# Performance work log

Measured on AMD Instinct MI355X. Metric: run time of the kernel, lower is better.

The kernel has to match this reference:

```python
import jax, jax.numpy as jnp
import numpy as np

# Model config (matches init_kwargs)
B, J, D_IN, D_MODEL, NUM_HEADS, NUM_LAYERS = 1024, 24, 64, 512, 8, 6
A = J + 1  # joints + cls token
LN_EPS = 1e-5


def setup_inputs() -> dict:
    key = jax.random.key(0)
    ks = jax.random.split(key, 14)
    s = 0.02  # weight init scale
    return {
        "x": jax.random.normal(ks[0], (B, J, D_IN), dtype=jnp.float32),
        # per-joint input embeddings: Linear(d_in, d_model) x J
        "We": jax.random.normal(ks[1], (J, D_IN, D_MODEL), dtype=jnp.float32) * s,
        "be": jnp.zeros((J, D_MODEL), dtype=jnp.float32),
        "cls_token": jax.random.normal(ks[2], (D_MODEL,), dtype=jnp.float32),
        # per-layer shared key/value projections
        "Wk": jax.random.normal(ks[3], (NUM_LAYERS, D_MODEL, D_MODEL), dtype=jnp.float32) * s,
        "bk": jnp.zeros((NUM_LAYERS, D_MODEL), dtype=jnp.float32),
        "Wv": jax.random.normal(ks[4], (NUM_LAYERS, D_MODEL, D_MODEL), dtype=jnp.float32) * s,
        "bv": jnp.zeros((NUM_LAYERS, D_MODEL), dtype=jnp.float32),
        # per-layer, PER-JOINT query projections (ModuleList of A linears)
        "Wq": jax.random.normal(ks[5], (NUM_LAYERS, A, D_MODEL, D_MODEL), dtype=jnp.float32) * s,
        "bq": jnp.zeros((NUM_LAYERS, A, D_MODEL), dtype=jnp.float32),
        "Wo": jax.random.normal(ks[6], (NUM_LAYERS, D_MODEL, D_MODEL), dtype=jnp.float32) * s,
        "bo": jnp.zeros((NUM_LAYERS, D_MODEL), dtype=jnp.float32),
        "ln_g": jnp.ones((NUM_LAYERS, D_MODEL), dtype=jnp.float32),
        "ln_b": jnp.zeros((NUM_LAYERS, D_MODEL), dtype=jnp.float32),
    }


def _layernorm(y, g, b):
    m = jnp.mean(y, axis=-1, keepdims=True)
    v = jnp.var(y, axis=-1, keepdims=True)  # ddof=0 matches torch LayerNorm
    return (y - m) * jax.lax.rsqrt(v + LN_EPS) * g + b


def reference(x, We, be, cls_token, Wk, bk, Wv, bv, Wq, bq, Wo, bo, ln_g, ln_b):
    b = x.shape[0]
    depth = D_MODEL // NUM_HEADS
    # per-joint input embedding -> (B, J, D)
    tok = jnp.einsum("bjd,jde->bje", x, We) + be
    cls = jnp.broadcast_to(cls_token[None, None, :], (b, 1, D_MODEL))
    h = jnp.concatenate([cls, tok], axis=1)  # (B, A, D); the seq dim of 1 is dropped

    def split(t):  # (B, A, D) -> (B, H, A, depth)
        return t.reshape(b, A, NUM_HEADS, depth).transpose(0, 2, 1, 3)

    for l in range(NUM_LAYERS):
        k = h @ Wk[l] + bk[l]                                  # (B, A, D)
        v = h @ Wv[l] + bv[l]                                  # (B, A, D)
        q = jnp.einsum("bad,ade->bae", h, Wq[l]) + bq[l]        # per-joint query
        qh, kh, vh = split(q), split(k), split(v)
        scores = jnp.einsum("bhqd,bhkd->bhqk", qh, kh) / jnp.sqrt(jnp.float32(depth))
        w = jax.nn.softmax(scores, axis=-1)                    # (B, H, A, A)
        o = jnp.einsum("bhqk,bhkd->bhqd", w, vh)
        o = o.transpose(0, 2, 1, 3).reshape(b, A, D_MODEL)
        o = o @ Wo[l] + bo[l]
        h = _layernorm(h + o, ln_g[l], ln_b[l])
    return h  # (B, A, D) == inputs[:, 0, :, :] in the torch code
```

## Files before the change

### kernel.cpp

```cpp
#include <hip/hip_runtime.h>

typedef unsigned short u16;
typedef unsigned int u32;
typedef short bf16x8 __attribute__((ext_vector_type(8)));
typedef float f32x4 __attribute__((ext_vector_type(4)));

#define AS1 __attribute__((address_space(1)))
#define AS3 __attribute__((address_space(3)))

__device__ __forceinline__ u16 f2b(float f) {
  u32 u = __float_as_uint(f);
  u += 0x7fffu + ((u >> 16) & 1u);
  return (u16)(u >> 16);
}
__device__ __forceinline__ float b2f(u16 s) {
  return __uint_as_float(((u32)s) << 16);
}

__device__ __forceinline__ void gload16(const u16* g, u16* l) {
  __builtin_amdgcn_global_load_lds((const AS1 void*)g, (AS3 void*)l, 16, 0, 0);
}

__global__ __launch_bounds__(256) void prep_kernel(const float* __restrict__ x,
                                                   const float* __restrict__ cls,
                                                   u16* __restrict__ xb,
                                                   u16* __restrict__ hb) {
  if (blockIdx.x < 1536) {
    int i = blockIdx.x * 256 + threadIdx.x;
    float4 v = ((const float4*)x)[i];
    ushort4 u;
    u.x = f2b(v.x); u.y = f2b(v.y); u.z = f2b(v.z); u.w = f2b(v.w);
    ((ushort4*)xb)[i] = u;
  } else {
    int i = (blockIdx.x - 1536) * 256 + threadIdx.x;
    int b = i >> 7;
    int e = (i & 127) << 2;
    float4 v = *(const float4*)(cls + e);
    long off = (long)b * (25 * 512) + e;
    ushort4 u;
    u.x = f2b(v.x); u.y = f2b(v.y); u.z = f2b(v.z); u.w = f2b(v.w);
    *(ushort4*)(hb + off) = u;
  }
}

__device__ __forceinline__ void conv_tile(const float* __restrict__ src,
                                          u16* __restrict__ dst,
                                          int K, int N, int k0, int n0,
                                          void* smem) {
  float (*t)[65] = (float(*)[65])smem;
  for (int i = threadIdx.x; i < 4096; i += 256) {
    int r = i >> 6, c = i & 63;
    t[r][c] = src[(long)(k0 + r) * N + n0 + c];
  }
  __syncthreads();
  for (int i = threadIdx.x; i < 4096; i += 256) {
    int r = i >> 6, c = i & 63;
    dst[(long)(n0 + r) * K + k0 + c] = f2b(t[c][r]);
  }
}

__global__ __launch_bounds__(256) void convT_kernel(const float* __restrict__ src,
                                                    u16* __restrict__ dst,
                                                    int K, int N,
                                                    long src_gstride, long dst_gstride) {
  __shared__ float t[64][65];
  conv_tile(src + (long)blockIdx.z * src_gstride, dst + (long)blockIdx.z * dst_gstride,
            K, N, blockIdx.x * 64, blockIdx.y * 64, t);
}

__global__ __launch_bounds__(256) void convT4_kernel(
    const float* __restrict__ wq, const float* __restrict__ wk,
    const float* __restrict__ wv, const float* __restrict__ wo,
    u16* __restrict__ dq, u16* __restrict__ dk,
    u16* __restrict__ dv, u16* __restrict__ dwo) {
  __shared__ float t[64][65];
  const int z = blockIdx.z;
  const float* src;
  u16* dst;
  if (z < 25)      { src = wq + (long)z * 262144; dst = dq + (long)z * 262144; }
  else if (z == 25){ src = wk; dst = dk; }
  else if (z == 26){ src = wv; dst = dv; }
  else             { src = wo; dst = dwo; }
  conv_tile(src, dst, 512, 512, blockIdx.x * 64, blockIdx.y * 64, t);
}

__device__ __forceinline__ void gemm_core(u16* lds,
    const u16* Ag, long a_stride, const u16* Wg, const float* biasg,
    u16* Cg, long c_stride, int K, int m0, int n0) {
  u16* As = lds;
  u16* Bs = lds + 8192;

  const int tid = threadIdx.x;
  const int lane = tid & 63;
  const int wave = tid >> 6;
  const int wr = wave >> 1, wc = wave & 1;

  const int schunk = lane & 7;
  const u16* ga[4];
  const u16* gb[4];
  int lo[4];
#pragma unroll
  for (int i = 0; i < 4; ++i) {
    const int r = wave * 32 + i * 8 + (lane >> 3);
    const int csw = (schunk ^ (r & 7)) << 3;
    ga[i] = Ag + (long)(m0 + r) * a_stride + csw;
    gb[i] = Wg + (long)(n0 + r) * K + csw;
    lo[i] = (wave * 32 + i * 8) * 64;
  }

  f32x4 acc[4][4];
#pragma unroll
  for (int m = 0; m < 4; ++m)
#pragma unroll
    for (int n = 0; n < 4; ++n) {
      acc[m][n][0] = 0.f; acc[m][n][1] = 0.f;
      acc[m][n][2] = 0.f; acc[m][n][3] = 0.f;
    }

  const int nt = K >> 6;
  for (int t = 0; t < nt; ++t) {
    const int k0 = t << 6;
#pragma unroll
    for (int i = 0; i < 4; ++i) {
      gload16(ga[i] + k0, As + lo[i]);
      gload16(gb[i] + k0, Bs + lo[i]);
    }
    __syncthreads();

#pragma unroll
    for (int kk = 0; kk < 64; kk += 32) {
      const int kb = kk + ((lane >> 4) << 3);
      bf16x8 af[4], bfr[4];
#pragma unroll
      for (int m = 0; m < 4; ++m) {
        const int R = (wr << 6) + (m << 4) + (lane & 15);
        af[m] = *(const bf16x8*)&As[((R << 6) + kb) ^ ((R & 7) << 3)];
      }
#pragma unroll
      for (int n = 0; n < 4; ++n) {
        const int Cc = (wc << 6) + (n << 4) + (lane & 15);
        bfr[n] = *(const bf16x8*)&Bs[((Cc << 6) + kb) ^ ((Cc & 7) << 3)];
      }
#pragma unroll
      for (int m = 0; m < 4; ++m)
#pragma unroll
        for (int n = 0; n < 4; ++n)
          acc[m][n] = __builtin_amdgcn_mfma_f32_16x16x32_bf16(af[m], bfr[n],
                                                              acc[m][n], 0, 0, 0);
    }
    if (t + 1 < nt) __syncthreads();
  }

  const int lcol = lane & 15;
  const int lrow = (lane >> 4) << 2;
#pragma unroll
  for (int n = 0; n < 4; ++n) {
    const int col = n0 + (wc << 6) + (n << 4) + lcol;
    const float bv = biasg[col];
#pragma unroll
    for (int m = 0; m < 4; ++m) {
      const int row = m0 + (wr << 6) + (m << 4) + lrow;
#pragma unroll
      for (int j = 0; j < 4; ++j) {
        const float val = acc[m][n][j] + bv;
        Cg[(long)(row + j) * c_stride + col] = f2b(val);
      }
    }
  }
}

__global__ __launch_bounds__(256) void gemm_plain(
    const u16* __restrict__ Abase, long a_stride, long a_goff,
    const u16* __restrict__ Wbase, long w_gstride,
    const float* __restrict__ biasbase, long bias_gstride,
    u16* __restrict__ Cb, long c_stride, long c_goff, int K) {
  __shared__ u16 lds[16384];
  const int gx = gridDim.x, gy = gridDim.y;
  int lin = blockIdx.x + gx * (blockIdx.y + gy * blockIdx.z);
  const int total = gx * gy * gridDim.z;
  const int chunk = total >> 3;
  lin = (lin & 7) * chunk + (lin >> 3);
  const int g = lin / (gx * gy);
  const int rem = lin % (gx * gy);
  const int mt = rem % gx;
  const int nt = rem / gx;
  gemm_core(lds,
            Abase + (long)g * a_goff, a_stride,
            Wbase + (long)g * w_gstride,
            biasbase + (long)g * bias_gstride,
            Cb + (long)g * c_goff, c_stride, K,
            mt * 128, nt * 128);
}

__global__ __launch_bounds__(256) void gemm_qkv(
    const u16* __restrict__ hb,
    const u16* __restrict__ wqT, const u16* __restrict__ wkT, const u16* __restrict__ wvT,
    const float* __restrict__ bq, const float* __restrict__ bk, const float* __restrict__ bv,
    u16* __restrict__ qb, u16* __restrict__ kb, u16* __restrict__ vb) {
  __shared__ u16 lds[16384];
  const int bid = (blockIdx.x & 7) * 300 + (blockIdx.x >> 3);
  const u16* Ag; long a_str; const u16* Wg; const float* bg; u16* Cg; long c_str;
  int mt, nt;
  if (bid < 800) {
    const int g = bid >> 5, rem = bid & 31;
    mt = rem >> 2; nt = rem & 3;
    Ag = hb + (long)g * 512; a_str = 12800;
    Wg = wqT + (long)g * 262144; bg = bq + (long)g * 512;
    Cg = qb + (long)g * 512; c_str = 12800;
  } else if (bid < 1600) {
    const int rem = bid - 800;
    mt = rem >> 2; nt = rem & 3;
    Ag = hb; a_str = 512; Wg = wkT; bg = bk; Cg = kb; c_str = 512;
  } else {
    const int rem = bid - 1600;
    mt = rem >> 2; nt = rem & 3;
    Ag = hb; a_str = 512; Wg = wvT; bg = bv; Cg = vb; c_str = 512;
  }
  gemm_core(lds, Ag, a_str, Wg, bg, Cg, c_str, 512, mt * 128, nt * 128);
}

__global__ __launch_bounds__(256) void attn_kernel(const u16* __restrict__ q,
                                                   u16* __restrict__ kio,
                                                   const u16* __restrict__ v) {
  __shared__ float ks_[25 * 256];
  __shared__ float vs_[25 * 256];
  const int tid = threadIdx.x;
  const int b = blockIdx.x >> 1;
  const int h0 = blockIdx.x & 1;
  const long base = (long)b * 25 * 512;

  for (int i = tid; i < 800; i += 256) {
    const int j = i >> 5, c = i & 31;
    const long goff = base + (long)j * 512 + h0 * 256 + c * 8;
    uint4 kt = *(const uint4*)(kio + goff);
    uint4 vt = *(const uint4*)(v + goff);
    const u32 ka[4] = {kt.x, kt.y, kt.z, kt.w};
    const u32 va[4] = {vt.x, vt.y, vt.z, vt.w};
    float4 k0f = {b2f((u16)ka[0]), b2f((u16)(ka[0] >> 16)),
                  b2f((u16)ka[1]), b2f((u16)(ka[1] >> 16))};
    float4 k1f = {b2f((u16)ka[2]), b2f((u16)(ka[2] >> 16)),
                  b2f((u16)ka[3]), b2f((u16)(ka[3] >> 16))};
    float4 v0f = {b2f((u16)va[0]), b2f((u16)(va[0] >> 16)),
                  b2f((u16)va[1]), b2f((u16)(va[1] >> 16))};
    float4 v1f = {b2f((u16)va[2]), b2f((u16)(va[2] >> 16)),
                  b2f((u16)va[3]), b2f((u16)(va[3] >> 16))};
    const int off = j * 256 + c * 8;
    *(float4*)&ks_[off]     = k0f;
    *(float4*)&ks_[off + 4] = k1f;
    *(float4*)&vs_[off]     = v0f;
    *(float4*)&vs_[off + 4] = v1f;
  }
  __syncthreads();

  const int w = tid >> 6;
  const int lane = tid & 63;
  const int qi = lane >> 1;
  const int half = lane & 1;
  if (qi < 25) {
    const int h = h0 * 4 + w;
    const int dslice = w * 64 + half * 32;

    const u16* qrow = q + base + (long)qi * 512 + h * 64 + half * 32;
    float buf[32];
#pragma unroll
    for (int c = 0; c < 4; ++c) {
      uint4 t = *(const uint4*)(qrow + c * 8);
      const u32 tt[4] = {t.x, t.y, t.z, t.w};
#pragma unroll
      for (int e = 0; e < 4; ++e) {
        buf[c * 8 + 2 * e]     = b2f((u16)tt[e]);
        buf[c * 8 + 2 * e + 1] = b2f((u16)(tt[e] >> 16));
      }
    }

    float sc[25];
    float mx = -1e30f;
#pragma unroll
    for (int j = 0; j < 25; ++j) {
      const float4* kr = (const float4*)&ks_[j * 256 + dslice];
      float s0 = 0.f, s1 = 0.f;
#pragma unroll
      for (int c4 = 0; c4 < 8; ++c4) {
        float4 kv = kr[c4];
        s0 += buf[4 * c4 + 0] * kv.x + buf[4 * c4 + 1] * kv.y;
        s1 += buf[4 * c4 + 2] * kv.z + buf[4 * c4 + 3] * kv.w;
      }
      float s = s0 + s1;
      s += __shfl_xor(s, 1);
      s *= 0.125f;
      sc[j] = s;
      mx = fmaxf(mx, s);
    }
    float sum = 0.f;
#pragma unroll
    for (int j = 0; j < 25; ++j) {
      sc[j] = __expf(sc[j] - mx);
      sum += sc[j];
    }
    const float inv = 1.f / sum;

#pragma unroll
    for (int d = 0; d < 32; ++d) buf[d] = 0.f;
#pragma unroll
    for (int j = 0; j < 25; ++j) {
      const float wj = sc[j];
      const float4* vr = (const float4*)&vs_[j * 256 + dslice];
#pragma unroll
      for (int c4 = 0; c4 < 8; ++c4) {
        float4 vv = vr[c4];
        buf[4 * c4 + 0] += wj * vv.x;
        buf[4 * c4 + 1] += wj * vv.y;
        buf[4 * c4 + 2] += wj * vv.z;
        buf[4 * c4 + 3] += wj * vv.w;
      }
    }

    u16* orow = kio + base + (long)qi * 512 + h * 64 + half * 32;
#pragma unroll
    for (int c = 0; c < 4; ++c) {
      uint4 t;
      u32 tt[4];
#pragma unroll
      for (int e = 0; e < 4; ++e)
        tt[e] = (u32)f2b(buf[c * 8 + 2 * e] * inv) |
                ((u32)f2b(buf[c * 8 + 2 * e + 1] * inv) << 16);
      t.x = tt[0]; t.y = tt[1]; t.z = tt[2]; t.w = tt[3];
      *(uint4*)(orow + c * 8) = t;
    }
  }
}

__global__ __launch_bounds__(256) void ln_kernel(u16* hb,
                                                 const u16* __restrict__ o,
                                                 const float* __restrict__ g,
                                                 const float* __restrict__ bta,
                                                 float* fout) {
  const int lane = threadIdx.x & 63;
  const int wave = threadIdx.x >> 6;
  const long row = (long)blockIdx.x * 4 + wave;
  u16* hr = hb + row * 512;
  const u16* orow = o + row * 512;
  const int base = lane << 3;
  uint4 hv4 = *(const uint4*)(hr + base);
  uint4 ov = *(const uint4*)(orow + base);
  const u32 ha[4] = {hv4.x, hv4.y, hv4.z, hv4.w};
  const u32 oa[4] = {ov.x, ov.y, ov.z, ov.w};
  float y[8];
#pragma unroll
  for (int e = 0; e < 4; ++e) {
    y[2 * e]     = b2f((u16)ha[e])         + b2f((u16)oa[e]);
    y[2 * e + 1] = b2f((u16)(ha[e] >> 16)) + b2f((u16)(oa[e] >> 16));
  }
  float s = 0.f, ss = 0.f;
#pragma unroll
  for (int i = 0; i < 8; ++i) { s += y[i]; ss += y[i] * y[i]; }
#pragma unroll
  for (int off = 32; off > 0; off >>= 1) {
    s += __shfl_down(s, off);
    ss += __shfl_down(ss, off);
  }
  s = __shfl(s, 0);
  ss = __shfl(ss, 0);
  const float mean = s * (1.f / 512.f);
  const float var = ss * (1.f / 512.f) - mean * mean;
  const float rinv = rsqrtf(var + 1e-5f);
  float4 g0 = *(const float4*)(g + base);
  float4 g1 = *(const float4*)(g + base + 4);
  float4 b0 = *(const float4*)(bta + base);
  float4 b1 = *(const float4*)(bta + base + 4);
  float r[8];
  r[0] = (y[0] - mean) * rinv * g0.x + b0.x;
  r[1] = (y[1] - mean) * rinv * g0.y + b0.y;
  r[2] = (y[2] - mean) * rinv * g0.z + b0.z;
  r[3] = (y[3] - mean) * rinv * g0.w + b0.w;
  r[4] = (y[4] - mean) * rinv * g1.x + b1.x;
  r[5] = (y[5] - mean) * rinv * g1.y + b1.y;
  r[6] = (y[6] - mean) * rinv * g1.z + b1.z;
  r[7] = (y[7] - mean) * rinv * g1.w + b1.w;
  uint4 hv;
  hv.x = (u32)f2b(r[0]) | ((u32)f2b(r[1]) << 16);
  hv.y = (u32)f2b(r[2]) | ((u32)f2b(r[3]) << 16);
  hv.z = (u32)f2b(r[4]) | ((u32)f2b(r[5]) << 16);
  hv.w = (u32)f2b(r[6]) | ((u32)f2b(r[7]) << 16);
  *(uint4*)(hr + base) = hv;
  if (fout) {
    float* fr = fout + row * 512 + base;
    float4 w0 = {r[0], r[1], r[2], r[3]};
    float4 w1 = {r[4], r[5], r[6], r[7]};
    *(float4*)(fr) = w0;
    *(float4*)(fr + 4) = w1;
  }
}

extern "C" void kernel_launch(void* const* d_in, const int* in_sizes, int n_in,
                              void* d_out, int out_size, void* d_ws, size_t ws_size,
                              hipStream_t stream) {
  const float* x   = (const float*)d_in[0];
  const float* We  = (const float*)d_in[1];
  const float* be  = (const float*)d_in[2];
  const float* cls = (const float*)d_in[3];
  const float* Wk  = (const float*)d_in[4];
  const float* bk  = (const float*)d_in[5];
  const float* Wv  = (const float*)d_in[6];
  const float* bv  = (const float*)d_in[7];
  const float* Wq  = (const float*)d_in[8];
  const float* bq  = (const float*)d_in[9];
  const float* Wo  = (const float*)d_in[10];
  const float* bo  = (const float*)d_in[11];
  const float* lng = (const float*)d_in[12];
  const float* lnb = (const float*)d_in[13];
  float* out = (float*)d_out;

  char* ws = (char*)d_ws;
  u16* hb = (u16*)ws;
  u16* kb = (u16*)(ws + 26214400);
  u16* vb = (u16*)(ws + 52428800);
  u16* qb = (u16*)(ws + 78643200);
  u16* xb = kb;

  u16* scr = (u16*)d_out;
  u16* weT = scr + 7340032;
  u16* wqT = scr;
  u16* wkT = scr + 6553600;
  u16* wvT = scr + 6815744;
  u16* woT = scr + 7077888;

  prep_kernel<<<2048, 256, 0, stream>>>(x, cls, xb, hb);
  convT_kernel<<<dim3(1, 8, 24), 256, 0, stream>>>(We, weT, 64, 512, 32768, 32768);
  gemm_plain<<<dim3(8, 4, 24), 256, 0, stream>>>(
      xb, 1536, 64, weT, 32768, be, 512, hb + 512, 12800, 512, 64);

  for (int l = 0; l < 6; ++l) {
    convT4_kernel<<<dim3(8, 8, 28), 256, 0, stream>>>(
        Wq + (long)l * 6553600, Wk + (long)l * 262144,
        Wv + (long)l * 262144, Wo + (long)l * 262144,
        wqT, wkT, wvT, woT);
    gemm_qkv<<<2400, 256, 0, stream>>>(
        hb, wqT, wkT, wvT,
        bq + (long)l * 12800, bk + (long)l * 512, bv + (long)l * 512,
        qb, kb, vb);
    attn_kernel<<<2048, 256, 0, stream>>>(qb, kb, vb);
    gemm_plain<<<dim3(200, 4, 1), 256, 0, stream>>>(
        kb, 512, 0, woT, 0, bo + (long)l * 512, 0, qb, 512, 0, 512);
    ln_kernel<<<6400, 256, 0, stream>>>(hb, qb, lng + l * 512, lnb + l * 512,
                                        (l == 5) ? out : nullptr);
  }
}
```

Before: 1.027 ms.

## Fuse K/V projections sharing A tiles and fuse output projection with LayerNorm

K and V projections now share each loaded tile of h in one block, computing both accumulators, which halves A-tile loads and the block count for that part. A new gemm_oln kernel computes the full 512-wide output-projection row block with 512 threads, stages the result in LDS, then applies the residual add and LayerNorm in place. This removes the intermediate projection write/read and a separate launch for layers 0-4, while the last layer keeps the old path to write the fp32 output. The cost is higher register pressure (two accumulator sets) and more LDS per block, which may reduce occupancy.

```diff
diff --git a/kernel.cpp b/kernel.cpp
--- a/kernel.cpp
+++ b/kernel.cpp
@@ -164,6 +164,97 @@
       for (int j = 0; j < 4; ++j) {
         const float val = acc[m][n][j] + bv;
         Cg[(long)(row + j) * c_stride + col] = f2b(val);
+      }
+    }
+  }
+}
+
+__device__ __forceinline__ void kv_core(u16* lds,
+    const u16* Ag, const u16* Wk, const u16* Wv,
+    const float* bbk, const float* bbv,
+    u16* Ck, u16* Cv, int m0, int n0) {
+  u16* As = lds;
+  u16* Bk = lds + 8192;
+  u16* Bv = lds + 16384;
+
+  const int tid = threadIdx.x;
+  const int lane = tid & 63;
+  const int wave = tid >> 6;
+  const int wr = wave >> 1, wc = wave & 1;
+
+  const int schunk = lane & 7;
+  int aoff[4], boff[4], lo[4];
+#pragma unroll
+  for (int i = 0; i < 4; ++i) {
+    const int r = wave * 32 + i * 8 + (lane >> 3);
+    const int csw = (schunk ^ (r & 7)) << 3;
+    aoff[i] = (m0 + r) * 512 + csw;
+    boff[i] = (n0 + r) * 512 + csw;
+    lo[i] = (wave * 32 + i * 8) * 64;
+  }
+
+  f32x4 ak[4][4], av[4][4];
+#pragma unroll
+  for (int m = 0; m < 4; ++m)
+#pragma unroll
+    for (int n = 0; n < 4; ++n) {
+      ak[m][n][0] = 0.f; ak[m][n][1] = 0.f; ak[m][n][2] = 0.f; ak[m][n][3] = 0.f;
+      av[m][n][0] = 0.f; av[m][n][1] = 0.f; av[m][n][2] = 0.f; av[m][n][3] = 0.f;
+    }
+
+  for (int t = 0; t < 8; ++t) {
+    const int k0 = t << 6;
+#pragma unroll
+    for (int i = 0; i < 4; ++i) {
+      gload16(Ag + aoff[i] + k0, As + lo[i]);
+      gload16(Wk + boff[i] + k0, Bk + lo[i]);
+      gload16(Wv + boff[i] + k0, Bv + lo[i]);
+    }
+    __syncthreads();
+
+#pragma unroll
+    for (int kk = 0; kk < 64; kk += 32) {
+      const int kb = kk + ((lane >> 4) << 3);
+      bf16x8 af[4], bkf[4], bvf[4];
+#pragma unroll
+      for (int m = 0; m < 4; ++m) {
+        const int R = (wr << 6) + (m << 4) + (lane & 15);
+        af[m] = *(const bf16x8*)&As[((R << 6) + kb) ^ ((R & 7) << 3)];
+      }
+#pragma unroll
+      for (int n = 0; n < 4; ++n) {
+        const int Cc = (wc << 6) + (n << 4) + (lane & 15);
+        bkf[n] = *(const bf16x8*)&Bk[((Cc << 6) + kb) ^ ((Cc & 7) << 3)];
+        bvf[n] = *(const bf16x8*)&Bv[((Cc << 6) + kb) ^ ((Cc & 7) << 3)];
+      }
+#pragma unroll
+      for (int m = 0; m < 4; ++m)
+#pragma unroll
+        for (int n = 0; n < 4; ++n) {
+          ak[m][n] = __builtin_amdgcn_mfma_f32_16x16x32_bf16(af[m], bkf[n],
+                                                             ak[m][n], 0, 0, 0);
+          av[m][n] = __builtin_amdgcn_mfma_f32_16x16x32_bf16(af[m], bvf[n],
+                                                             av[m][n], 0, 0, 0);
+        }
+    }
+    if (t < 7) __syncthreads();
+  }
+
+  const int lcol = lane & 15;
+  const int lrow = (lane >> 4) << 2;
+#pragma unroll
+  for (int n = 0; n < 4; ++n) {
+    const int col = n0 + (wc << 6) + (n << 4) + lcol;
+    const float bvk = bbk[col];
+    const float bvv = bbv[col];
+#pragma unroll
+    for (int m = 0; m < 4; ++m) {
+      const int row = m0 + (wr << 6) + (m << 4) + lrow;
+#pragma unroll
+      for (int j = 0; j < 4; ++j) {
+        const long off = (long)(row + j) * 512 + col;
+        Ck[off] = f2b(ak[m][n][j] + bvk);
+        Cv[off] = f2b(av[m][n][j] + bvv);
       }
     }
   }
@@ -197,26 +288,19 @@
     const u16* __restrict__ wqT, const u16* __restrict__ wkT, const u16* __restrict__ wvT,
     const float* __restrict__ bq, const float* __restrict__ bk, const float* __restrict__ bv,
     u16* __restrict__ qb, u16* __restrict__ kb, u16* __restrict__ vb) {
-  __shared__ u16 lds[16384];
-  const int bid = (blockIdx.x & 7) * 300 + (blockIdx.x >> 3);
-  const u16* Ag; long a_str; const u16* Wg; const float* bg; u16* Cg; long c_str;
-  int mt, nt;
+  __shared__ u16 lds[3 * 8192];
+  const int bid = (blockIdx.x & 7) * 200 + (blockIdx.x >> 3);
   if (bid < 800) {
     const int g = bid >> 5, rem = bid & 31;
-    mt = rem >> 2; nt = rem & 3;
-    Ag = hb + (long)g * 512; a_str = 12800;
-    Wg = wqT + (long)g * 262144; bg = bq + (long)g * 512;
-    Cg = qb + (long)g * 512; c_str = 12800;
-  } else if (bid < 1600) {
+    const int mt = rem >> 2, nt = rem & 3;
+    gemm_core(lds, hb + (long)g * 512, 12800, wqT + (long)g * 262144,
+              bq + (long)g * 512, qb + (long)g * 512, 12800, 512,
+              mt * 128, nt * 128);
+  } else {
     const int rem = bid - 800;
-    mt = rem >> 2; nt = rem & 3;
-    Ag = hb; a_str = 512; Wg = wkT; bg = bk; Cg = kb; c_str = 512;
-  } else {
-    const int rem = bid - 1600;
-    mt = rem >> 2; nt = rem & 3;
-    Ag = hb; a_str = 512; Wg = wvT; bg = bv; Cg = vb; c_str = 512;
-  }
-  gemm_core(lds, Ag, a_str, Wg, bg, Cg, c_str, 512, mt * 128, nt * 128);
+    const int mt = rem >> 2, nt = rem & 3;
+    kv_core(lds, hb, wkT, wvT, bk, bv, kb, vb, mt * 128, nt * 128);
+  }
 }
 
 __global__ __launch_bounds__(256) void attn_kernel(const u16* __restrict__ q,
@@ -327,6 +411,141 @@
       t.x = tt[0]; t.y = tt[1]; t.z = tt[2]; t.w = tt[3];
       *(uint4*)(orow + c * 8) = t;
     }
+  }
+}
+
+__global__ __launch_bounds__(512) void gemm_oln(
+    const u16* __restrict__ ao,
+    const u16* __restrict__ woT,
+    const float* __restrict__ bo,
+    u16* __restrict__ hb,
+    const float* __restrict__ gam, const float* __restrict__ bet) {
+  __shared__ u16 As[4096];
+  __shared__ u16 Bs[32768];
+  const int tid = threadIdx.x;
+  const int lane = tid & 63;
+  const int wave = tid >> 6;
+  const int mb = (int)(blockIdx.x & 7) * 50 + (int)(blockIdx.x >> 3);
+  const int m0 = mb * 64;
+
+  const int sr = tid >> 3;
+  const int schunk = ((tid & 7) ^ (sr & 7)) << 3;
+  const int aoff = (m0 + sr) * 512 + schunk;
+  int boff[8];
+#pragma unroll
+  for (int i = 0; i < 8; ++i) boff[i] = (i * 64 + sr) * 512 + schunk;
+  const int lA = (wave << 3) << 6;
+  int lB[8];
+#pragma unroll
+  for (int i = 0; i < 8; ++i) lB[i] = ((i * 64 + (wave << 3))) << 6;
+
+  f32x4 acc[4][4];
+#pragma unroll
+  for (int m = 0; m < 4; ++m)
+#pragma unroll
+    for (int n = 0; n < 4; ++n) {
+      acc[m][n][0] = 0.f; acc[m][n][1] = 0.f;
+      acc[m][n][2] = 0.f; acc[m][n][3] = 0.f;
+    }
+
+  for (int t = 0; t < 8; ++t) {
+    const int k0 = t << 6;
+    gload16(ao + aoff + k0, As + lA);
+#pragma unroll
+    for (int i = 0; i < 8; ++i) gload16(woT + boff[i] + k0, Bs + lB[i]);
+    __syncthreads();
+
+#pragma unroll
+    for (int kk = 0; kk < 64; kk += 32) {
+      const int kb = kk + ((lane >> 4) << 3);
+      bf16x8 af[4], bfr[4];
+#pragma unroll
+      for (int m = 0; m < 4; ++m) {
+        const int R = (m << 4) + (lane & 15);
+        af[m] = *(const bf16x8*)&As[((R << 6) + kb) ^ ((R & 7) << 3)];
+      }
+#pragma unroll
+      for (int n = 0; n < 4; ++n) {
+        const int Cc = (wave << 6) + (n << 4) + (lane & 15);
+        bfr[n] = *(const bf16x8*)&Bs[((Cc << 6) + kb) ^ ((Cc & 7) << 3)];
+      }
+#pragma unroll
+      for (int m = 0; m < 4; ++m)
+#pragma unroll
+        for (int n = 0; n < 4; ++n)
+          acc[m][n] = __builtin_amdgcn_mfma_f32_16x16x32_bf16(af[m], bfr[n],
+                                                              acc[m][n], 0, 0, 0);
+    }
+    __syncthreads();
+  }
+
+  u16* C = Bs;
+  {
+    const int lcol = lane & 15;
+    const int lrow = (lane >> 4) << 2;
+#pragma unroll
+    for (int n = 0; n < 4; ++n) {
+      const int col = (wave << 6) + (n << 4) + lcol;
+      const float bv = bo[col];
+#pragma unroll
+      for (int m = 0; m < 4; ++m) {
+#pragma unroll
+        for (int j = 0; j < 4; ++j) {
+          const int row = (m << 4) + lrow + j;
+          C[((row << 9) + col) ^ ((row & 7) << 3)] = f2b(acc[m][n][j] + bv);
+        }
+      }
+    }
+  }
+  __syncthreads();
+
+  const int ebase = lane << 3;
+#pragma unroll
+  for (int rr = 0; rr < 8; ++rr) {
+    const int row = (rr << 3) + wave;
+    uint4 cv = *(const uint4*)&C[((row << 9) + ebase) ^ ((row & 7) << 3)];
+    const long grow = (long)(m0 + row) * 512;
+    uint4 hv4 = *(const uint4*)(hb + grow + ebase);
+    const u32 ha[4] = {hv4.x, hv4.y, hv4.z, hv4.w};
+    const u32 oa[4] = {cv.x, cv.y, cv.z, cv.w};
+    float y[8];
+#pragma unroll
+    for (int e = 0; e < 4; ++e) {
+      y[2 * e]     = b2f((u16)ha[e])         + b2f((u16)oa[e]);
+      y[2 * e + 1] = b2f((u16)(ha[e] >> 16)) + b2f((u16)(oa[e] >> 16));
+    }
+    float s = 0.f, ss = 0.f;
+#pragma unroll
+    for (int i = 0; i < 8; ++i) { s += y[i]; ss += y[i] * y[i]; }
+#pragma unroll
+    for (int off = 32; off > 0; off >>= 1) {
+      s += __shfl_down(s, off);
+      ss += __shfl_down(ss, off);
+    }
+    s = __shfl(s, 0);
+    ss = __shfl(ss, 0);
+    const float mean = s * (1.f / 512.f);
+    const float var = ss * (1.f / 512.f) - mean * mean;
+    const float rinv = rsqrtf(var + 1e-5f);
+    float4 g0 = *(const float4*)(gam + ebase);
+    float4 g1 = *(const float4*)(gam + ebase + 4);
+    float4 b0 = *(const float4*)(bet + ebase);
+    float4 b1 = *(const float4*)(bet + ebase + 4);
+    float r[8];
+    r[0] = (y[0] - mean) * rinv * g0.x + b0.x;
+    r[1] = (y[1] - mean) * rinv * g0.y + b0.y;
+    r[2] = (y[2] - mean) * rinv * g0.z + b0.z;
+    r[3] = (y[3] - mean) * rinv * g0.w + b0.w;
+    r[4] = (y[4] - mean) * rinv * g1.x + b1.x;
+    r[5] = (y[5] - mean) * rinv * g1.y + b1.y;
+    r[6] = (y[6] - mean) * rinv * g1.z + b1.z;
+    r[7] = (y[7] - mean) * rinv * g1.w + b1.w;
+    uint4 hv;
+    hv.x = (u32)f2b(r[0]) | ((u32)f2b(r[1]) << 16);
+    hv.y = (u32)f2b(r[2]) | ((u32)f2b(r[3]) << 16);
+    hv.z = (u32)f2b(r[4]) | ((u32)f2b(r[5]) << 16);
+    hv.w = (u32)f2b(r[6]) | ((u32)f2b(r[7]) << 16);
+    *(uint4*)(hb + grow + ebase) = hv;
   }
 }
 
@@ -435,14 +654,19 @@
         Wq + (long)l * 6553600, Wk + (long)l * 262144,
         Wv + (long)l * 262144, Wo + (long)l * 262144,
         wqT, wkT, wvT, woT);
-    gemm_qkv<<<2400, 256, 0, stream>>>(
+    gemm_qkv<<<1600, 256, 0, stream>>>(
         hb, wqT, wkT, wvT,
         bq + (long)l * 12800, bk + (long)l * 512, bv + (long)l * 512,
         qb, kb, vb);
     attn_kernel<<<2048, 256, 0, stream>>>(qb, kb, vb);
-    gemm_plain<<<dim3(200, 4, 1), 256, 0, stream>>>(
-        kb, 512, 0, woT, 0, bo + (long)l * 512, 0, qb, 512, 0, 512);
-    ln_kernel<<<6400, 256, 0, stream>>>(hb, qb, lng + l * 512, lnb + l * 512,
-                                        (l == 5) ? out : nullptr);
-  }
-}
+    if (l < 5) {
+      gemm_oln<<<400, 512, 0, stream>>>(
+          kb, woT, bo + (long)l * 512, hb,
+          lng + (long)l * 512, lnb + (long)l * 512);
+    } else {
+      gemm_plain<<<dim3(200, 4, 1), 256, 0, stream>>>(
+          kb, 512, 0, woT, 0, bo + (long)l * 512, 0, qb, 512, 0, 512);
+      ln_kernel<<<6400, 256, 0, stream>>>(hb, qb, lng + l * 512, lnb + l * 512, out);
+    }
+  }
+}
```

Result: slower. 1.314 ms (+27.9%).
